# Kernel optimization log

Measured on AMD Instinct MI355X. Metric: run time of the kernel, lower is better.

The kernel has to match this reference:

```python
import jax, jax.numpy as jnp
import numpy as np

B, T, D, O = 32, 1024, 1024, 256


def _glorot(key, shape):
    fan_in, fan_out = shape[0], shape[-1]
    std = np.sqrt(2.0 / (fan_in + fan_out))
    return jax.random.normal(key, shape, dtype=jnp.float32) * std


def setup_inputs() -> dict:
    key = jax.random.key(0)
    ks = jax.random.split(key, 14)
    return {
        "inputs": jax.random.normal(ks[0], (B, T, D), dtype=jnp.float32),
        # attention cell params
        "Wa": _glorot(ks[1], (O, O)),
        "Ua": _glorot(ks[2], (D, O)),
        "Va": _glorot(ks[3], (O, 1)),
        "Ba1": _glorot(ks[4], (1, O)),
        "Ba2": _glorot(ks[5], (T, O)),
        "Ba3": _glorot(ks[6], (T, 1)),
        # cascaded GRU cell params (Bo1 and inner keras GRUCell are unused in call)
        "Wo": _glorot(ks[7], (O, 1)),
        "Uo": _glorot(ks[8], (D, O)),
        "Co": _glorot(ks[9], (D, O)),
        "Bo2": _glorot(ks[10], (1, O)),
        "Bo3": _glorot(ks[11], (1, O)),
        "Bo4": _glorot(ks[12], (1, O)),
        "emb": _glorot(ks[13], (O, O)),
    }


def reference(inputs, Wa, Ua, Va, Ba1, Ba2, Ba3, Wo, Uo, Co, Bo2, Bo3, Bo4, emb):
    # inputs: [B, T, D]
    # UaH is identical every decoder step in the original code -> hoist (same math).
    UaH = jnp.einsum("btd,do->bto", inputs, Ua) + Ba2          # [B,T,O]
    # prev_state at step t is inputs[:, t-1, :] with wraparound at t=0.
    prev_in = jnp.roll(inputs, 1, axis=1)                        # [B,T,D]
    UoH_all = jnp.einsum("btd,do->bto", prev_in, Uo) + Bo2      # [B,T,O]

    def step(prev_pred, uoh_t):
        # --- attention cell (query = tanh(prev_pred)) ---
        WaS = jnp.tanh(prev_pred) @ Wa + Ba1                     # [B,O]
        scores = jnp.tanh(UaH + WaS[:, None, :]) @ Va + Ba3     # [B,T,1]
        sm = jax.nn.softmax(scores, axis=1)                      # [B,T,1]
        ctx = jnp.sum(inputs * sm, axis=1)                       # [B,D]
        # --- cascaded GRU cell ---
        woy = (jax.nn.softmax(prev_pred) @ emb) @ Wo             # [B,1]
        coc = ctx @ Co + Bo3                                     # [B,O]
        pred = woy + uoh_t + coc + Bo4                           # [B,O]
        return pred, pred

    init = jnp.zeros((inputs.shape[0], Wa.shape[0]), dtype=inputs.dtype)
    _, outs = jax.lax.scan(step, init, jnp.swapaxes(UoH_all, 0, 1))  # [T,B,O]
    return jnp.swapaxes(outs, 0, 1)                                   # [B,T,O]
```

## Files before the change

### kernel.cpp

```cpp
#include <hip/hip_runtime.h>
#include <hip/hip_fp16.h>


typedef unsigned int uint32;
typedef unsigned short u16;

#define NTH 512

__device__ __forceinline__ float b2f(u16 u) { return __uint_as_float(((uint32)u) << 16); }
__device__ __forceinline__ u16 f2b(float f) {
    uint32 u = __float_as_uint(f);
    uint32 r = u + 0x7fffu + ((u >> 16) & 1u);
    return (u16)(r >> 16);
}
__device__ __forceinline__ float lo_bf(uint32 d) { return __uint_as_float(d << 16); }
__device__ __forceinline__ float hi_bf(uint32 d) { return __uint_as_float(d & 0xffff0000u); }
__device__ __forceinline__ float tanh_fast(float x) {
    float e = __expf(x + x);
    return 1.0f - 2.0f * __builtin_amdgcn_rcpf(e + 1.0f);
}

__device__ __forceinline__ uint32 coh_ld(const uint32* p) {
    return __hip_atomic_load(p, __ATOMIC_RELAXED, __HIP_MEMORY_SCOPE_AGENT);
}
__device__ __forceinline__ void coh_st(uint32* p, uint32 v) {
    __hip_atomic_store(p, v, __ATOMIC_RELAXED, __HIP_MEMORY_SCOPE_AGENT);
}

#define OFF_E  ((size_t)0)
#define OFF_IC ((size_t)16777216)
#define WS_NEEDED ((size_t)33554432)

__device__ uint32 g_Pf[2][32][8][264];
__device__ uint32 g_flag[2][32][8];
__device__ float g_embWo[256];

__global__ __launch_bounds__(512) void init_flags() {
    ((uint32*)g_flag)[threadIdx.x] = 0xFFFFFFFFu;
}

__global__ void setup_embWo(const float* __restrict__ emb, const float* __restrict__ Wo) {
    int o = threadIdx.x;
    float a = 0.f;
    for (int j = 0; j < 256; j++) a = fmaf(emb[o * 256 + j], Wo[j], a);
    g_embWo[o] = a;
}

__global__ __launch_bounds__(256) void gemm_pre(
    const float* __restrict__ in, const float* __restrict__ Ua,
    const float* __restrict__ Uo, const float* __restrict__ Co,
    const float* __restrict__ Ba2, const float* __restrict__ Bo2,
    const float* __restrict__ Bo3, const float* __restrict__ Bo4,
    u16* __restrict__ E, float* __restrict__ outStage, u16* __restrict__ ic) {
    __shared__ __align__(16) float smA[32][132];
    __shared__ __align__(16) float smB[32][128];

    int tid = threadIdx.x;
    int rt = blockIdx.x, ct = blockIdx.y;
    int mat = ct >> 1;
    int o0 = (ct & 1) * 128;
    const float* W = (mat == 0) ? Ua : (mat == 1 ? Uo : Co);
    int r0 = rt * 128;
    int b = r0 >> 10, t0 = r0 & 1023;
    int tr = tid >> 4, tc = tid & 15;

    float acc[8][8];
#pragma unroll
    for (int i = 0; i < 8; i++)
#pragma unroll
        for (int j = 0; j < 8; j++) acc[i][j] = 0.f;

    for (int kc = 0; kc < 1024; kc += 32) {
#pragma unroll
        for (int l = 0; l < 4; l++) {
            int s = tid + l * 256;
            int i = s >> 3, c = s & 7;
            float4 v = *(const float4*)(in + (size_t)(r0 + i) * 1024 + kc + c * 4);
            smA[c * 4 + 0][i] = v.x;
            smA[c * 4 + 1][i] = v.y;
            smA[c * 4 + 2][i] = v.z;
            smA[c * 4 + 3][i] = v.w;
        }
#pragma unroll
        for (int l = 0; l < 4; l++) {
            int s = tid + l * 256;
            int dd = s >> 5, c = s & 31;
            *(float4*)&smB[dd][c * 4] = *(const float4*)(W + (size_t)(kc + dd) * 256 + o0 + c * 4);
        }
        __syncthreads();
#pragma unroll 4
        for (int j = 0; j < 32; j++) {
            float a0[8], b0[8];
            *(float4*)&a0[0] = *(const float4*)&smA[j][tr * 8];
            *(float4*)&a0[4] = *(const float4*)&smA[j][tr * 8 + 4];
            *(float4*)&b0[0] = *(const float4*)&smB[j][tc * 8];
            *(float4*)&b0[4] = *(const float4*)&smB[j][tc * 8 + 4];
#pragma unroll
            for (int rr = 0; rr < 8; rr++)
#pragma unroll
                for (int cc = 0; cc < 8; cc++) acc[rr][cc] = fmaf(a0[rr], b0[cc], acc[rr][cc]);
        }
        __syncthreads();
    }

    if (mat == 0) {
#pragma unroll
        for (int rr = 0; rr < 8; rr++) {
            int t = t0 + tr * 8 + rr;
#pragma unroll
            for (int cc = 0; cc < 8; cc++) {
                int o = o0 + tc * 8 + cc;
                float v = __expf(2.f * (acc[rr][cc] + Ba2[t * 256 + o]));
                E[((((size_t)b << 10) + t) << 8) + o] = f2b(v);
            }
        }
    } else if (mat == 1) {
#pragma unroll
        for (int rr = 0; rr < 8; rr++) {
            int t = t0 + tr * 8 + rr;
            int t1 = (t + 1) & 1023;
#pragma unroll
            for (int cc = 0; cc < 8; cc++) {
                int o = o0 + tc * 8 + cc;
                outStage[(((size_t)b << 10) + t1) * 256 + o] = acc[rr][cc] + Bo2[o] + Bo3[o] + Bo4[o];
            }
        }
    } else {
#pragma unroll
        for (int rr = 0; rr < 8; rr++) {
            int t = t0 + tr * 8 + rr;
#pragma unroll
            for (int cc = 0; cc < 8; cc++)
                ic[(((size_t)b << 10) + t) * 256 + o0 + tc * 8 + cc] = f2b(acc[rr][cc]);
        }
    }
}

__global__ __launch_bounds__(NTH) void seq8(
    const float* __restrict__ Wa, const float* __restrict__ Va,
    const float* __restrict__ Ba1, const float* __restrict__ Ba3,
    const u16* __restrict__ E, const u16* __restrict__ IC,
    float* __restrict__ out) {
    __shared__ uint32 smWa2[128 * 256];
    __shared__ __align__(16) float smScratch[2064];
    __shared__ float smPred[256], smQ[256], smF[256], smVa[256], smBa1[256];
    __shared__ float smS[128], smEe[128], smBa3[128];
    __shared__ float smT[16];

    int tid = threadIdx.x;
    int b = blockIdx.x & 31, g = blockIdx.x >> 5;
    int lane = tid & 63, w = tid >> 6;
    int t0 = g << 7;

    if (tid < 256) {
        smVa[tid] = Va[tid]; smBa1[tid] = Ba1[tid];
        smPred[tid] = 0.f; smQ[tid] = 0.f;
    }
    if (tid < 128) smBa3[tid] = Ba3[t0 + tid];
    for (int idx = tid; idx < 32768; idx += NTH) {
        int j2 = idx >> 8, o = idx & 255;
        uint32 u0 = (uint32)f2b(Wa[(size_t)(2 * j2) * 256 + o]);
        uint32 u1 = (uint32)f2b(Wa[(size_t)(2 * j2 + 1) * 256 + o]);
        smWa2[idx] = u0 | (u1 << 16);
    }
    __syncthreads();

    float sv = (tid < 256) ? smVa[tid] : 0.f;
#pragma unroll
    for (int off = 32; off; off >>= 1) sv += __shfl_xor(sv, off, 64);
    if (lane == 0) smT[w] = sv;
    __syncthreads();
    float sumVa = smT[0] + smT[1] + smT[2] + smT[3];
    float myEmb = (tid < 256) ? g_embWo[tid] : 0.f;
    __syncthreads();

    const u16* Eb = E + ((size_t)b << 18);
    const u16* ICb = IC + ((size_t)b << 18);
    float* outb = out + ((size_t)b << 18);
    long bud = 1000000000L;

    for (int t = 0; t < 1024; t++) {
        uint32* bufP  = &g_Pf[t & 1][b][g][0];
        uint32* flags = &g_flag[t & 1][b][0];
        float uoh = (tid < 256) ? outb[((size_t)t << 8) + tid] : 0.f;

        float pv = 0.f;
        if (tid < 256) {
            pv = smPred[tid];
            float m = pv;
#pragma unroll
            for (int off = 32; off; off >>= 1) m = fmaxf(m, __shfl_xor(m, off, 64));
            if (lane == 0) smT[w] = m;
        }
        {
            int o = tid & 255, h = tid >> 8;
            const uint32* wp = &smWa2[(h << 6) * 256 + o];
            const float* qp = &smQ[h << 7];
            float a = 0.f;
#pragma unroll 8
            for (int j2 = 0; j2 < 64; j2++) {
                float2 q2 = *(const float2*)&qp[j2 * 2];
                uint32 p = wp[j2 << 8];
                a = fmaf(lo_bf(p), q2.x, a);
                a = fmaf(hi_bf(p), q2.y, a);
            }
            smScratch[tid] = a;
        }
        __syncthreads();
        if (tid < 256) {
            float M = fmaxf(fmaxf(smT[0], smT[1]), fmaxf(smT[2], smT[3]));
            float e = __expf(pv - M);
            float s1 = e, s2 = e * myEmb;
#pragma unroll
            for (int off = 32; off; off >>= 1) {
                s1 += __shfl_xor(s1, off, 64);
                s2 += __shfl_xor(s2, off, 64);
            }
            if (lane == 0) { smT[4 + w] = s1; smT[8 + w] = s2; }
            smF[tid] = __expf(2.f * (smBa1[tid] + smScratch[tid] + smScratch[256 + tid]));
        }
        __syncthreads();
        float p_val = (smT[8] + smT[9] + smT[10] + smT[11]) *
                      __builtin_amdgcn_rcpf(smT[4] + smT[5] + smT[6] + smT[7]);

        {
            int tl = tid >> 2, oq = tid & 3;
            const uint4* row = (const uint4*)(Eb + (((size_t)(t0 + tl)) << 8) + (oq << 6));
            float acc = 0.f;
#pragma unroll
            for (int k = 0; k < 8; k++) {
                int kk = (k + oq) & 7;
                uint4 ev = row[kk];
                int ob = (oq << 6) + (kk << 3);
                float4 fA = *(const float4*)&smF[ob];
                float4 fB = *(const float4*)&smF[ob + 4];
                float4 vA = *(const float4*)&smVa[ob];
                float4 vB = *(const float4*)&smVa[ob + 4];
                acc = fmaf(vA.x, __builtin_amdgcn_rcpf(fmaf(lo_bf(ev.x), fA.x, 1.f)), acc);
                acc = fmaf(vA.y, __builtin_amdgcn_rcpf(fmaf(hi_bf(ev.x), fA.y, 1.f)), acc);
                acc = fmaf(vA.z, __builtin_amdgcn_rcpf(fmaf(lo_bf(ev.y), fA.z, 1.f)), acc);
                acc = fmaf(vA.w, __builtin_amdgcn_rcpf(fmaf(hi_bf(ev.y), fA.w, 1.f)), acc);
                acc = fmaf(vB.x, __builtin_amdgcn_rcpf(fmaf(lo_bf(ev.z), fB.x, 1.f)), acc);
                acc = fmaf(vB.y, __builtin_amdgcn_rcpf(fmaf(hi_bf(ev.z), fB.y, 1.f)), acc);
                acc = fmaf(vB.z, __builtin_amdgcn_rcpf(fmaf(lo_bf(ev.w), fB.z, 1.f)), acc);
                acc = fmaf(vB.w, __builtin_amdgcn_rcpf(fmaf(hi_bf(ev.w), fB.w, 1.f)), acc);
            }
            acc += __shfl_xor(acc, 1, 64);
            acc += __shfl_xor(acc, 2, 64);
            if (oq == 0) smS[tl] = sumVa - 2.f * acc + smBa3[tl];
        }
        __syncthreads();
        float m_g = 0.f, S_g = 0.f;
        if (tid < 128) {
            float s = smS[tid];
            float mm = s;
#pragma unroll
            for (int off = 32; off; off >>= 1) mm = fmaxf(mm, __shfl_xor(mm, off, 64));
            if (lane == 0) smT[w] = mm;
        }
        __syncthreads();
        if (tid < 128) {
            m_g = fmaxf(smT[0], smT[1]);
            float e = __expf(smS[tid] - m_g);
            smEe[tid] = e;
            float ls = e;
#pragma unroll
            for (int off = 32; off; off >>= 1) ls += __shfl_xor(ls, off, 64);
            if (lane == 0) smT[2 + w] = ls;
        }
        __syncthreads();
        m_g = fmaxf(smT[0], smT[1]);
        S_g = smT[2] + smT[3];
        if (tid == 0) {
            coh_st(&bufP[256], __float_as_uint(m_g));
            coh_st(&bufP[257], __float_as_uint(S_g));
        }

        {
            int rg = tid >> 6, oc = tid & 63, o4 = oc << 2;
            const u16* icp = ICb + (((size_t)t0) << 8) + o4;
            float4 a4 = {0.f, 0.f, 0.f, 0.f};
#pragma unroll 4
            for (int r = 0; r < 16; r++) {
                int row = (rg << 4) + r;
                float e = smEe[row];
                uint2 iv = *(const uint2*)(icp + ((size_t)row << 8));
                a4.x = fmaf(e, lo_bf(iv.x), a4.x);
                a4.y = fmaf(e, hi_bf(iv.x), a4.y);
                a4.z = fmaf(e, lo_bf(iv.y), a4.z);
                a4.w = fmaf(e, hi_bf(iv.y), a4.w);
            }
            *(float4*)&smScratch[rg * 256 + o4] = a4;
        }
        __syncthreads();
        if (tid < 256) {
            float Pmine = 0.f;
#pragma unroll
            for (int rg = 0; rg < 8; rg++) Pmine += smScratch[rg * 256 + tid];
            coh_st(&bufP[tid], __float_as_uint(Pmine));
        }
        __syncthreads();
        if (tid == 0) coh_st(&flags[g], (uint32)t);
        if (tid < 8 && tid != g) {
            while (bud > 0) {
                if (atomicAdd(&flags[tid], 0u) == (uint32)t) break;
                bud--;
            }
        }
        __syncthreads();
        float p8[8];
        {
            const uint32* pb = &g_Pf[t & 1][b][0][0];
            if (tid < 256) {
#pragma unroll
                for (int g2 = 0; g2 < 8; g2++)
                    p8[g2] = __uint_as_float(coh_ld(&pb[g2 * 264 + tid]));
            } else if (tid < 256 + 16) {
                int i = tid & 15;
                smT[i] = __uint_as_float(coh_ld(&pb[(i >> 1) * 264 + 256 + (i & 1)]));
            }
        }
        __syncthreads();
        if (tid < 256) {
            float M = smT[0];
#pragma unroll
            for (int g2 = 1; g2 < 8; g2++) M = fmaxf(M, smT[2 * g2]);
            float L = 0.f, Pt = 0.f;
#pragma unroll
            for (int g2 = 0; g2 < 8; g2++) {
                float eg = __expf(smT[2 * g2] - M);
                L = fmaf(eg, smT[2 * g2 + 1], L);
                Pt = fmaf(eg, p8[g2], Pt);
            }
            float pr = p_val + uoh + Pt * __builtin_amdgcn_rcpf(L);
            if ((tid >> 5) == g) outb[((size_t)t << 8) + tid] = pr;
            smPred[tid] = pr;
            smQ[tid] = tanh_fast(pr);
        }
        __syncthreads();
    }
}

__global__ void zero_k(uint32* out, int n) {
    int i = blockIdx.x * 1024 + threadIdx.x;
    if (i < n) out[i] = 0;
}

extern "C" void kernel_launch(void* const* d_in, const int* in_sizes, int n_in,
                              void* d_out, int out_size, void* d_ws, size_t ws_size,
                              hipStream_t stream) {
    const float* in = (const float*)d_in[0];
    const float* Wa = (const float*)d_in[1];
    const float* Ua = (const float*)d_in[2];
    const float* Va = (const float*)d_in[3];
    const float* Ba1 = (const float*)d_in[4];
    const float* Ba2 = (const float*)d_in[5];
    const float* Ba3 = (const float*)d_in[6];
    const float* Wo = (const float*)d_in[7];
    const float* Uo = (const float*)d_in[8];
    const float* Co = (const float*)d_in[9];
    const float* Bo2 = (const float*)d_in[10];
    const float* Bo3 = (const float*)d_in[11];
    const float* Bo4 = (const float*)d_in[12];
    const float* emb = (const float*)d_in[13];
    float* out = (float*)d_out;
    char* ws = (char*)d_ws;

    if (ws_size < WS_NEEDED) {
        zero_k<<<(out_size + 1023) / 1024, 1024, 0, stream>>>((uint32*)out, out_size);
        return;
    }

    u16* E = (u16*)(ws + OFF_E);
    u16* icp = (u16*)(ws + OFF_IC);

    init_flags<<<1, 512, 0, stream>>>();
    setup_embWo<<<1, 256, 0, stream>>>(emb, Wo);
    gemm_pre<<<dim3(256, 6), 256, 0, stream>>>(in, Ua, Uo, Co, Ba2, Bo2, Bo3, Bo4, E, out, icp);
    seq8<<<256, NTH, 0, stream>>>(Wa, Va, Ba1, Ba3, E, icp, out);
}
```

Baseline: 6.948 ms.

## Cache E/IC tiles in registers, fp16-pack cross-block partials, merge softmax reductions

Loads each thread's E and IC tile slices into registers once before the time loop instead of reloading them from global memory every step. The cross-block partial context sums and the (max, sum) pairs are packed to fp16 pairs, which halves the coherent exchange traffic, and the flag-wait and read phases are merged to drop a barrier. The local softmax is reduced within one wavefront over two elements per lane, which removes two block barriers. The trade is higher register pressure (about 40 extra VGPRs) and fp16 precision loss in the partial sums and the max/sum values, which could affect accuracy and may overflow for large exponent sums.

```diff
diff --git a/kernel.cpp b/kernel.cpp
--- a/kernel.cpp
+++ b/kernel.cpp
@@ -4,6 +4,7 @@
 
 typedef unsigned int uint32;
 typedef unsigned short u16;
+typedef unsigned long long u64;
 
 #define NTH 512
 
@@ -19,8 +20,21 @@
     float e = __expf(x + x);
     return 1.0f - 2.0f * __builtin_amdgcn_rcpf(e + 1.0f);
 }
+__device__ __forceinline__ uint32 pack2h(float x, float y) {
+    return (uint32)__half_as_ushort(__float2half(x)) |
+           ((uint32)__half_as_ushort(__float2half(y)) << 16);
+}
+__device__ __forceinline__ float unpk_lo(uint32 w) {
+    return __half2float(__ushort_as_half((unsigned short)(w & 0xFFFFu)));
+}
+__device__ __forceinline__ float unpk_hi(uint32 w) {
+    return __half2float(__ushort_as_half((unsigned short)(w >> 16)));
+}
 
 __device__ __forceinline__ uint32 coh_ld(const uint32* p) {
+    return __hip_atomic_load(p, __ATOMIC_RELAXED, __HIP_MEMORY_SCOPE_AGENT);
+}
+__device__ __forceinline__ u64 coh_ld64(const u64* p) {
     return __hip_atomic_load(p, __ATOMIC_RELAXED, __HIP_MEMORY_SCOPE_AGENT);
 }
 __device__ __forceinline__ void coh_st(uint32* p, uint32 v) {
@@ -31,7 +45,8 @@
 #define OFF_IC ((size_t)16777216)
 #define WS_NEEDED ((size_t)33554432)
 
-__device__ uint32 g_Pf[2][32][8][264];
+__device__ uint32 g_Ph[2][32][8][132];
+__device__ uint32 g_mS[2][32][8];
 __device__ uint32 g_flag[2][32][8];
 __device__ float g_embWo[256];
 
@@ -142,7 +157,7 @@
     const u16* __restrict__ E, const u16* __restrict__ IC,
     float* __restrict__ out) {
     __shared__ uint32 smWa2[128 * 256];
-    __shared__ __align__(16) float smScratch[2064];
+    __shared__ __align__(16) float smScratch[2048];
     __shared__ float smPred[256], smQ[256], smF[256], smVa[256], smBa1[256];
     __shared__ float smS[128], smEe[128], smBa3[128];
     __shared__ float smT[16];
@@ -179,8 +194,24 @@
     float* outb = out + ((size_t)b << 18);
     long bud = 1000000000L;
 
+    uint4 ev8[8];
+    {
+        int tl = tid >> 2, oq = tid & 3;
+        const uint4* row = (const uint4*)(Eb + (((size_t)(t0 + tl)) << 8) + (oq << 6));
+#pragma unroll
+        for (int k = 0; k < 8; k++) ev8[k] = row[(k + oq) & 7];
+    }
+    uint2 icv[16];
+    {
+        int rg = tid >> 6, o4 = (tid & 63) << 2;
+        const u16* icp = ICb + (((size_t)t0) << 8) + o4;
+#pragma unroll
+        for (int r = 0; r < 16; r++)
+            icv[r] = *(const uint2*)(icp + ((size_t)((rg << 4) + r) << 8));
+    }
+
     for (int t = 0; t < 1024; t++) {
-        uint32* bufP  = &g_Pf[t & 1][b][g][0];
+        uint32* bufP  = &g_Ph[t & 1][b][g][0];
         uint32* flags = &g_flag[t & 1][b][0];
         float uoh = (tid < 256) ? outb[((size_t)t << 8) + tid] : 0.f;
 
@@ -225,13 +256,11 @@
 
         {
             int tl = tid >> 2, oq = tid & 3;
-            const uint4* row = (const uint4*)(Eb + (((size_t)(t0 + tl)) << 8) + (oq << 6));
             float acc = 0.f;
 #pragma unroll
             for (int k = 0; k < 8; k++) {
-                int kk = (k + oq) & 7;
-                uint4 ev = row[kk];
-                int ob = (oq << 6) + (kk << 3);
+                uint4 ev = ev8[k];
+                int ob = (oq << 6) + (((k + oq) & 7) << 3);
                 float4 fA = *(const float4*)&smF[ob];
                 float4 fB = *(const float4*)&smF[ob + 4];
                 float4 vA = *(const float4*)&smVa[ob];
@@ -250,41 +279,26 @@
             if (oq == 0) smS[tl] = sumVa - 2.f * acc + smBa3[tl];
         }
         __syncthreads();
-        float m_g = 0.f, S_g = 0.f;
-        if (tid < 128) {
-            float s = smS[tid];
-            float mm = s;
+        if (tid < 64) {
+            float s0 = smS[tid], s1 = smS[tid + 64];
+            float mm = fmaxf(s0, s1);
 #pragma unroll
             for (int off = 32; off; off >>= 1) mm = fmaxf(mm, __shfl_xor(mm, off, 64));
-            if (lane == 0) smT[w] = mm;
-        }
-        __syncthreads();
-        if (tid < 128) {
-            m_g = fmaxf(smT[0], smT[1]);
-            float e = __expf(smS[tid] - m_g);
-            smEe[tid] = e;
-            float ls = e;
+            float e0 = __expf(s0 - mm), e1 = __expf(s1 - mm);
+            smEe[tid] = e0; smEe[tid + 64] = e1;
+            float ls = e0 + e1;
 #pragma unroll
             for (int off = 32; off; off >>= 1) ls += __shfl_xor(ls, off, 64);
-            if (lane == 0) smT[2 + w] = ls;
-        }
-        __syncthreads();
-        m_g = fmaxf(smT[0], smT[1]);
-        S_g = smT[2] + smT[3];
-        if (tid == 0) {
-            coh_st(&bufP[256], __float_as_uint(m_g));
-            coh_st(&bufP[257], __float_as_uint(S_g));
-        }
-
+            if (tid == 0) coh_st(&g_mS[t & 1][b][g], pack2h(mm, ls));
+        }
+        __syncthreads();
         {
-            int rg = tid >> 6, oc = tid & 63, o4 = oc << 2;
-            const u16* icp = ICb + (((size_t)t0) << 8) + o4;
+            int rg = tid >> 6, o4 = (tid & 63) << 2;
             float4 a4 = {0.f, 0.f, 0.f, 0.f};
 #pragma unroll 4
             for (int r = 0; r < 16; r++) {
-                int row = (rg << 4) + r;
-                float e = smEe[row];
-                uint2 iv = *(const uint2*)(icp + ((size_t)row << 8));
+                float e = smEe[(rg << 4) + r];
+                uint2 iv = icv[r];
                 a4.x = fmaf(e, lo_bf(iv.x), a4.x);
                 a4.y = fmaf(e, hi_bf(iv.x), a4.y);
                 a4.z = fmaf(e, lo_bf(iv.y), a4.z);
@@ -293,11 +307,14 @@
             *(float4*)&smScratch[rg * 256 + o4] = a4;
         }
         __syncthreads();
-        if (tid < 256) {
-            float Pmine = 0.f;
-#pragma unroll
-            for (int rg = 0; rg < 8; rg++) Pmine += smScratch[rg * 256 + tid];
-            coh_st(&bufP[tid], __float_as_uint(Pmine));
+        if (tid < 128) {
+            float px = 0.f, py = 0.f;
+#pragma unroll
+            for (int rg = 0; rg < 8; rg++) {
+                float2 v = *(const float2*)&smScratch[rg * 256 + 2 * tid];
+                px += v.x; py += v.y;
+            }
+            coh_st(&bufP[tid], pack2h(px, py));
         }
         __syncthreads();
         if (tid == 0) coh_st(&flags[g], (uint32)t);
@@ -308,29 +325,29 @@
             }
         }
         __syncthreads();
-        float p8[8];
-        {
-            const uint32* pb = &g_Pf[t & 1][b][0][0];
-            if (tid < 256) {
-#pragma unroll
-                for (int g2 = 0; g2 < 8; g2++)
-                    p8[g2] = __uint_as_float(coh_ld(&pb[g2 * 264 + tid]));
-            } else if (tid < 256 + 16) {
-                int i = tid & 15;
-                smT[i] = __uint_as_float(coh_ld(&pb[(i >> 1) * 264 + 256 + (i & 1)]));
-            }
-        }
-        __syncthreads();
         if (tid < 256) {
-            float M = smT[0];
-#pragma unroll
-            for (int g2 = 1; g2 < 8; g2++) M = fmaxf(M, smT[2 * g2]);
+            const uint32* pb = &g_Ph[t & 1][b][0][0];
+            int wo = tid >> 1, hsel = tid & 1;
+            uint32 pw[8];
+#pragma unroll
+            for (int g2 = 0; g2 < 8; g2++) pw[g2] = coh_ld(&pb[g2 * 132 + wo]);
+            const u64* msp = (const u64*)&g_mS[t & 1][b][0];
+            u64 q0 = coh_ld64(&msp[0]), q1 = coh_ld64(&msp[1]);
+            u64 q2 = coh_ld64(&msp[2]), q3 = coh_ld64(&msp[3]);
+            uint32 msw[8] = {(uint32)q0, (uint32)(q0 >> 32),
+                             (uint32)q1, (uint32)(q1 >> 32),
+                             (uint32)q2, (uint32)(q2 >> 32),
+                             (uint32)q3, (uint32)(q3 >> 32)};
+            float M = unpk_lo(msw[0]);
+#pragma unroll
+            for (int g2 = 1; g2 < 8; g2++) M = fmaxf(M, unpk_lo(msw[g2]));
             float L = 0.f, Pt = 0.f;
 #pragma unroll
             for (int g2 = 0; g2 < 8; g2++) {
-                float eg = __expf(smT[2 * g2] - M);
-                L = fmaf(eg, smT[2 * g2 + 1], L);
-                Pt = fmaf(eg, p8[g2], Pt);
+                float eg = __expf(unpk_lo(msw[g2]) - M);
+                L = fmaf(eg, unpk_hi(msw[g2]), L);
+                float pg = hsel ? unpk_hi(pw[g2]) : unpk_lo(pw[g2]);
+                Pt = fmaf(eg, pg, Pt);
             }
             float pr = p_val + uoh + Pt * __builtin_amdgcn_rcpf(L);
             if ((tid >> 5) == g) outb[((size_t)t << 8) + tid] = pr;
```

Result: slower. 7.922 ms (+14.0%).

## Replace flag barrier with step-tagged fp16 payload words polled directly

Applied to the files above, without the earlier changes.

Each cross-block partial value (P, max, sum) is packed as fp16 with the step index in the upper 16 bits, so consumers poll the data words themselves instead of waiting on a separate flag and then reloading. This removes a block barrier, the flag store and the second round of coherent loads on every sequential step. In exchange, partial sums drop to fp16 precision, which risks accuracy loss or overflow, and every consumer thread now spins on nine coherent loads.

```diff
diff --git a/kernel.cpp b/kernel.cpp
--- a/kernel.cpp
+++ b/kernel.cpp
@@ -19,6 +19,12 @@
     float e = __expf(x + x);
     return 1.0f - 2.0f * __builtin_amdgcn_rcpf(e + 1.0f);
 }
+__device__ __forceinline__ uint32 packh(float f, int t) {
+    return (((uint32)t) << 16) | (uint32)__half_as_ushort(__float2half(f));
+}
+__device__ __forceinline__ float unpackh(uint32 w) {
+    return __half2float(__ushort_as_half((unsigned short)(w & 0xFFFFu)));
+}
 
 __device__ __forceinline__ uint32 coh_ld(const uint32* p) {
     return __hip_atomic_load(p, __ATOMIC_RELAXED, __HIP_MEMORY_SCOPE_AGENT);
@@ -31,12 +37,17 @@
 #define OFF_IC ((size_t)16777216)
 #define WS_NEEDED ((size_t)33554432)
 
-__device__ uint32 g_Pf[2][32][8][264];
-__device__ uint32 g_flag[2][32][8];
+__device__ uint32 g_P[2][32][8][264];
+__device__ uint32 g_mSt[2][32][16];
 __device__ float g_embWo[256];
 
-__global__ __launch_bounds__(512) void init_flags() {
-    ((uint32*)g_flag)[threadIdx.x] = 0xFFFFFFFFu;
+#define NP_WORDS (2 * 32 * 8 * 264)
+#define NMS_WORDS (2 * 32 * 16)
+
+__global__ __launch_bounds__(256) void init_k() {
+    int i = blockIdx.x * 256 + threadIdx.x;
+    if (i < NP_WORDS) ((uint32*)g_P)[i] = 0xFFFF0000u;
+    else ((uint32*)g_mSt)[i - NP_WORDS] = 0xFFFF0000u;
 }
 
 __global__ void setup_embWo(const float* __restrict__ emb, const float* __restrict__ Wo) {
@@ -142,7 +153,7 @@
     const u16* __restrict__ E, const u16* __restrict__ IC,
     float* __restrict__ out) {
     __shared__ uint32 smWa2[128 * 256];
-    __shared__ __align__(16) float smScratch[2064];
+    __shared__ __align__(16) float smScratch[2048];
     __shared__ float smPred[256], smQ[256], smF[256], smVa[256], smBa1[256];
     __shared__ float smS[128], smEe[128], smBa3[128];
     __shared__ float smT[16];
@@ -180,8 +191,8 @@
     long bud = 1000000000L;
 
     for (int t = 0; t < 1024; t++) {
-        uint32* bufP  = &g_Pf[t & 1][b][g][0];
-        uint32* flags = &g_flag[t & 1][b][0];
+        uint32* bufP = &g_P[t & 1][b][g][0];
+        uint32* msb  = &g_mSt[t & 1][b][0];
         float uoh = (tid < 256) ? outb[((size_t)t << 8) + tid] : 0.f;
 
         float pv = 0.f;
@@ -272,8 +283,8 @@
         m_g = fmaxf(smT[0], smT[1]);
         S_g = smT[2] + smT[3];
         if (tid == 0) {
-            coh_st(&bufP[256], __float_as_uint(m_g));
-            coh_st(&bufP[257], __float_as_uint(S_g));
+            coh_st(&msb[2 * g], packh(m_g, t));
+            coh_st(&msb[2 * g + 1], packh(S_g, t));
         }
 
         {
@@ -297,41 +308,52 @@
             float Pmine = 0.f;
 #pragma unroll
             for (int rg = 0; rg < 8; rg++) Pmine += smScratch[rg * 256 + tid];
-            coh_st(&bufP[tid], __float_as_uint(Pmine));
-        }
-        __syncthreads();
-        if (tid == 0) coh_st(&flags[g], (uint32)t);
-        if (tid < 8 && tid != g) {
+            coh_st(&bufP[tid], packh(Pmine, t));
+
+            const uint32* pb = &g_P[t & 1][b][0][0];
+            uint32 tt = (uint32)t;
+            uint32 w0 = 0xFFFF0000u, w1 = 0xFFFF0000u, w2 = 0xFFFF0000u,
+                   w3 = 0xFFFF0000u, w4 = 0xFFFF0000u, w5 = 0xFFFF0000u,
+                   w6 = 0xFFFF0000u, w7 = 0xFFFF0000u;
+            uint32 msv = (lane < 16) ? 0xFFFF0000u : (tt << 16);
             while (bud > 0) {
-                if (atomicAdd(&flags[tid], 0u) == (uint32)t) break;
+                if ((w0 >> 16) != tt) w0 = coh_ld(pb + 0 * 264 + tid);
+                if ((w1 >> 16) != tt) w1 = coh_ld(pb + 1 * 264 + tid);
+                if ((w2 >> 16) != tt) w2 = coh_ld(pb + 2 * 264 + tid);
+                if ((w3 >> 16) != tt) w3 = coh_ld(pb + 3 * 264 + tid);
+                if ((w4 >> 16) != tt) w4 = coh_ld(pb + 4 * 264 + tid);
+                if ((w5 >> 16) != tt) w5 = coh_ld(pb + 5 * 264 + tid);
+                if ((w6 >> 16) != tt) w6 = coh_ld(pb + 6 * 264 + tid);
+                if ((w7 >> 16) != tt) w7 = coh_ld(pb + 7 * 264 + tid);
+                if ((msv >> 16) != tt) msv = coh_ld(msb + (lane & 15));
+                bool done = ((w0 >> 16) == tt) && ((w1 >> 16) == tt) &&
+                            ((w2 >> 16) == tt) && ((w3 >> 16) == tt) &&
+                            ((w4 >> 16) == tt) && ((w5 >> 16) == tt) &&
+                            ((w6 >> 16) == tt) && ((w7 >> 16) == tt) &&
+                            ((msv >> 16) == tt);
+                if (__all(done)) break;
                 bud--;
             }
-        }
-        __syncthreads();
-        float p8[8];
-        {
-            const uint32* pb = &g_Pf[t & 1][b][0][0];
-            if (tid < 256) {
-#pragma unroll
-                for (int g2 = 0; g2 < 8; g2++)
-                    p8[g2] = __uint_as_float(coh_ld(&pb[g2 * 264 + tid]));
-            } else if (tid < 256 + 16) {
-                int i = tid & 15;
-                smT[i] = __uint_as_float(coh_ld(&pb[(i >> 1) * 264 + 256 + (i & 1)]));
-            }
-        }
-        __syncthreads();
-        if (tid < 256) {
-            float M = smT[0];
-#pragma unroll
-            for (int g2 = 1; g2 < 8; g2++) M = fmaxf(M, smT[2 * g2]);
-            float L = 0.f, Pt = 0.f;
-#pragma unroll
-            for (int g2 = 0; g2 < 8; g2++) {
-                float eg = __expf(smT[2 * g2] - M);
-                L = fmaf(eg, smT[2 * g2 + 1], L);
-                Pt = fmaf(eg, p8[g2], Pt);
-            }
+            float mg0 = unpackh(__shfl(msv, 0, 64)),  sg0 = unpackh(__shfl(msv, 1, 64));
+            float mg1 = unpackh(__shfl(msv, 2, 64)),  sg1 = unpackh(__shfl(msv, 3, 64));
+            float mg2 = unpackh(__shfl(msv, 4, 64)),  sg2 = unpackh(__shfl(msv, 5, 64));
+            float mg3 = unpackh(__shfl(msv, 6, 64)),  sg3 = unpackh(__shfl(msv, 7, 64));
+            float mg4 = unpackh(__shfl(msv, 8, 64)),  sg4 = unpackh(__shfl(msv, 9, 64));
+            float mg5 = unpackh(__shfl(msv, 10, 64)), sg5 = unpackh(__shfl(msv, 11, 64));
+            float mg6 = unpackh(__shfl(msv, 12, 64)), sg6 = unpackh(__shfl(msv, 13, 64));
+            float mg7 = unpackh(__shfl(msv, 14, 64)), sg7 = unpackh(__shfl(msv, 15, 64));
+            float M = fmaxf(fmaxf(fmaxf(mg0, mg1), fmaxf(mg2, mg3)),
+                            fmaxf(fmaxf(mg4, mg5), fmaxf(mg6, mg7)));
+            float e0 = __expf(mg0 - M), e1 = __expf(mg1 - M);
+            float e2 = __expf(mg2 - M), e3 = __expf(mg3 - M);
+            float e4 = __expf(mg4 - M), e5 = __expf(mg5 - M);
+            float e6 = __expf(mg6 - M), e7 = __expf(mg7 - M);
+            float L = e0 * sg0 + e1 * sg1 + e2 * sg2 + e3 * sg3 +
+                      e4 * sg4 + e5 * sg5 + e6 * sg6 + e7 * sg7;
+            float Pt = e0 * unpackh(w0) + e1 * unpackh(w1) +
+                       e2 * unpackh(w2) + e3 * unpackh(w3) +
+                       e4 * unpackh(w4) + e5 * unpackh(w5) +
+                       e6 * unpackh(w6) + e7 * unpackh(w7);
             float pr = p_val + uoh + Pt * __builtin_amdgcn_rcpf(L);
             if ((tid >> 5) == g) outb[((size_t)t << 8) + tid] = pr;
             smPred[tid] = pr;
@@ -374,7 +396,7 @@
     u16* E = (u16*)(ws + OFF_E);
     u16* icp = (u16*)(ws + OFF_IC);
 
-    init_flags<<<1, 512, 0, stream>>>();
+    init_k<<<532, 256, 0, stream>>>();
     setup_embWo<<<1, 256, 0, stream>>>(emb, Wo);
     gemm_pre<<<dim3(256, 6), 256, 0, stream>>>(in, Ua, Uo, Co, Ba2, Bo2, Bo3, Bo4, E, out, icp);
     seq8<<<256, NTH, 0, stream>>>(Wa, Va, Ba1, Ba3, E, icp, out);
```

Measured after the change: 7.387 ms. 6.3% more time.

## Replace per-step softmax max with a static score bound to drop syncs

Applied to the files above, without the earlier changes.

Since tanh is bounded, every score is at most sum|Va| + max(Ba3), so a constant offset is computed once in setup and used in place of the running softmax max. This removes the per-group max reduction, two block barriers, and the cross-group max/rescale merge in each of the 1024 sequential steps; groups now exchange only partial sums. The risk is underflow, since scores far below the bound give tiny or zero exponentials and the sum could lose precision or become zero.

```diff
diff --git a/kernel.cpp b/kernel.cpp
--- a/kernel.cpp
+++ b/kernel.cpp
@@ -34,16 +34,25 @@
 __device__ uint32 g_Pf[2][32][8][264];
 __device__ uint32 g_flag[2][32][8];
 __device__ float g_embWo[256];
+__device__ float g_M0;
 
 __global__ __launch_bounds__(512) void init_flags() {
     ((uint32*)g_flag)[threadIdx.x] = 0xFFFFFFFFu;
 }
 
-__global__ void setup_embWo(const float* __restrict__ emb, const float* __restrict__ Wo) {
+__global__ void setup_misc(const float* __restrict__ emb, const float* __restrict__ Wo,
+                           const float* __restrict__ Va, const float* __restrict__ Ba3) {
     int o = threadIdx.x;
     float a = 0.f;
     for (int j = 0; j < 256; j++) a = fmaf(emb[o * 256 + j], Wo[j], a);
     g_embWo[o] = a;
+    if (o == 0) {
+        float sa = 0.f;
+        for (int j = 0; j < 256; j++) sa += fabsf(Va[j]);
+        float mb = Ba3[0];
+        for (int j = 1; j < 1024; j++) mb = fmaxf(mb, Ba3[j]);
+        g_M0 = sa + mb + 1.0f;
+    }
 }
 
 __global__ __launch_bounds__(256) void gemm_pre(
@@ -142,10 +151,10 @@
     const u16* __restrict__ E, const u16* __restrict__ IC,
     float* __restrict__ out) {
     __shared__ uint32 smWa2[128 * 256];
-    __shared__ __align__(16) float smScratch[2064];
+    __shared__ __align__(16) float smScratch[2048];
     __shared__ float smPred[256], smQ[256], smF[256], smVa[256], smBa1[256];
-    __shared__ float smS[128], smEe[128], smBa3[128];
-    __shared__ float smT[16];
+    __shared__ float smEe[128], smBa3[128];
+    __shared__ float smT[24];
 
     int tid = threadIdx.x;
     int b = blockIdx.x & 31, g = blockIdx.x >> 5;
@@ -172,6 +181,7 @@
     __syncthreads();
     float sumVa = smT[0] + smT[1] + smT[2] + smT[3];
     float myEmb = (tid < 256) ? g_embWo[tid] : 0.f;
+    float M0 = g_M0;
     __syncthreads();
 
     const u16* Eb = E + ((size_t)b << 18);
@@ -247,34 +257,15 @@
             }
             acc += __shfl_xor(acc, 1, 64);
             acc += __shfl_xor(acc, 2, 64);
-            if (oq == 0) smS[tl] = sumVa - 2.f * acc + smBa3[tl];
-        }
-        __syncthreads();
-        float m_g = 0.f, S_g = 0.f;
-        if (tid < 128) {
-            float s = smS[tid];
-            float mm = s;
-#pragma unroll
-            for (int off = 32; off; off >>= 1) mm = fmaxf(mm, __shfl_xor(mm, off, 64));
-            if (lane == 0) smT[w] = mm;
-        }
-        __syncthreads();
-        if (tid < 128) {
-            m_g = fmaxf(smT[0], smT[1]);
-            float e = __expf(smS[tid] - m_g);
-            smEe[tid] = e;
-            float ls = e;
+            float score = sumVa - 2.f * acc + smBa3[tl];
+            float e = __expf(score - M0);
+            if (oq == 0) smEe[tl] = e;
+            float ls = (oq == 0) ? e : 0.f;
 #pragma unroll
             for (int off = 32; off; off >>= 1) ls += __shfl_xor(ls, off, 64);
-            if (lane == 0) smT[2 + w] = ls;
-        }
-        __syncthreads();
-        m_g = fmaxf(smT[0], smT[1]);
-        S_g = smT[2] + smT[3];
-        if (tid == 0) {
-            coh_st(&bufP[256], __float_as_uint(m_g));
-            coh_st(&bufP[257], __float_as_uint(S_g));
-        }
+            if (lane == 0) smT[16 + w] = ls;
+        }
+        __syncthreads();
 
         {
             int rg = tid >> 6, oc = tid & 63, o4 = oc << 2;
@@ -299,6 +290,11 @@
             for (int rg = 0; rg < 8; rg++) Pmine += smScratch[rg * 256 + tid];
             coh_st(&bufP[tid], __float_as_uint(Pmine));
         }
+        if (tid == 0) {
+            float S_g = smT[16] + smT[17] + smT[18] + smT[19] +
+                        smT[20] + smT[21] + smT[22] + smT[23];
+            coh_st(&bufP[256], __float_as_uint(S_g));
+        }
         __syncthreads();
         if (tid == 0) coh_st(&flags[g], (uint32)t);
         if (tid < 8 && tid != g) {
@@ -308,30 +304,18 @@
             }
         }
         __syncthreads();
-        float p8[8];
-        {
+        if (tid < 256) {
             const uint32* pb = &g_Pf[t & 1][b][0][0];
-            if (tid < 256) {
-#pragma unroll
-                for (int g2 = 0; g2 < 8; g2++)
-                    p8[g2] = __uint_as_float(coh_ld(&pb[g2 * 264 + tid]));
-            } else if (tid < 256 + 16) {
-                int i = tid & 15;
-                smT[i] = __uint_as_float(coh_ld(&pb[(i >> 1) * 264 + 256 + (i & 1)]));
-            }
-        }
-        __syncthreads();
-        if (tid < 256) {
-            float M = smT[0];
-#pragma unroll
-            for (int g2 = 1; g2 < 8; g2++) M = fmaxf(M, smT[2 * g2]);
-            float L = 0.f, Pt = 0.f;
-#pragma unroll
-            for (int g2 = 0; g2 < 8; g2++) {
-                float eg = __expf(smT[2 * g2] - M);
-                L = fmaf(eg, smT[2 * g2 + 1], L);
-                Pt = fmaf(eg, p8[g2], Pt);
-            }
+            float Pt = 0.f;
+#pragma unroll
+            for (int g2 = 0; g2 < 8; g2++)
+                Pt += __uint_as_float(coh_ld(&pb[g2 * 264 + tid]));
+            uint32 sown = 0;
+            if (lane < 8) sown = coh_ld(&pb[lane * 264 + 256]);
+            float L = 0.f;
+#pragma unroll
+            for (int g2 = 0; g2 < 8; g2++)
+                L += __uint_as_float(__shfl(sown, g2, 64));
             float pr = p_val + uoh + Pt * __builtin_amdgcn_rcpf(L);
             if ((tid >> 5) == g) outb[((size_t)t << 8) + tid] = pr;
             smPred[tid] = pr;
@@ -375,7 +359,7 @@
     u16* icp = (u16*)(ws + OFF_IC);
 
     init_flags<<<1, 512, 0, stream>>>();
-    setup_embWo<<<1, 256, 0, stream>>>(emb, Wo);
+    setup_misc<<<1, 256, 0, stream>>>(emb, Wo, Va, Ba3);
     gemm_pre<<<dim3(256, 6), 256, 0, stream>>>(in, Ua, Uo, Co, Ba2, Bo2, Bo3, Bo4, E, out, icp);
     seq8<<<256, NTH, 0, stream>>>(Wa, Va, Ba1, Ba3, E, icp, out);
 }
```

Result: faster. 6.677 ms (-3.9%).
